# Kernel optimization log

Measured on AMD Instinct MI355X. Metric: run time of the kernel, lower is better.

The kernel has to match this reference:

```python
import jax, jax.numpy as jnp
import numpy as np

N = 100000   # nodes
G = 256      # graphs
E = 120000   # edges per relation
IN = 162
HID = 128
R = 5
L = 2        # extra RGCN layers beyond the initial one


def setup_inputs() -> dict:
    key = jax.random.key(0)
    ks = jax.random.split(key, 24)
    s = 0.05
    inp = {
        "X": jax.random.normal(ks[0], (N, IN), jnp.float32),
        "batch": jnp.sort(jax.random.randint(ks[6], (N,), 0, G)),
    }
    for i in range(R):
        inp[f"edge_index{i+1}"] = jax.random.randint(ks[1 + i], (2, E), 0, N)
    # RGCN initial layer params
    inp["W0"] = jax.random.normal(ks[7], (R, IN, HID), jnp.float32) * s
    inp["root0"] = jax.random.normal(ks[8], (IN, HID), jnp.float32) * s
    inp["b0"] = jnp.zeros((HID,), jnp.float32)
    # stacked params for the L hidden RGCN layers
    inp["Wl"] = jax.random.normal(ks[9], (L, R, HID, HID), jnp.float32) * s
    inp["rootl"] = jax.random.normal(ks[10], (L, HID, HID), jnp.float32) * s
    inp["bl"] = jnp.zeros((L, HID), jnp.float32)
    # classification head
    inp["Wc1"] = jax.random.normal(ks[11], (HID, HID), jnp.float32) * s
    inp["bc1"] = jnp.zeros((HID,), jnp.float32)
    inp["Wc2"] = jax.random.normal(ks[12], (HID, HID), jnp.float32) * s
    inp["bc2"] = jnp.zeros((HID,), jnp.float32)
    inp["Wc3"] = jax.random.normal(ks[13], (HID, 1), jnp.float32) * s
    inp["bc3"] = jnp.zeros((1,), jnp.float32)
    return inp


def _seg_mean(msg, dst, num):
    # scatter-mean over destination nodes (PyG RGCNConv uses aggr='mean' per relation)
    s = jax.ops.segment_sum(msg, dst, num_segments=num)
    c = jax.ops.segment_sum(jnp.ones(msg.shape[0], msg.dtype), dst, num_segments=num)
    return s / jnp.maximum(c, 1.0)[:, None]


def _rgcn(x, W, root, b, src, dst):
    # src, dst: [R, E]; W: [R, d_in, d_out]
    msgs = jnp.einsum("ref,rfh->reh", x[src], W)          # [R, E, HID]
    agg = jax.vmap(_seg_mean, in_axes=(0, 0, None))(msgs, dst, N)  # [R, N, HID]
    return x @ root + b + agg.sum(0)


def reference(X, edge_index1, edge_index2, edge_index3, edge_index4, edge_index5,
              batch, W0, root0, b0, Wl, rootl, bl, Wc1, bc1, Wc2, bc2, Wc3, bc3):
    ei = jnp.stack([edge_index1, edge_index2, edge_index3, edge_index4, edge_index5])  # [R,2,E]
    src, dst = ei[:, 0, :], ei[:, 1, :]
    h = jax.nn.relu(_rgcn(X, W0, root0, b0, src, dst))
    for l in range(L):
        h = jax.nn.relu(_rgcn(h, Wl[l], rootl[l], bl[l], src, dst))
    # mean readout over graphs
    s = jax.ops.segment_sum(h, batch, num_segments=G)
    c = jax.ops.segment_sum(jnp.ones((N,), h.dtype), batch, num_segments=G)
    read = s / jnp.maximum(c, 1.0)[:, None]
    h = jax.nn.relu(read @ Wc1 + bc1)
    h = jax.nn.relu(h @ Wc2 + bc2)
    return h @ Wc3 + bc3
```

## Files before the change

### kernel.cpp

```cpp
#include <hip/hip_runtime.h>

#define N_NODES 100000
#define NPAD    100096
#define NTILES  782
#define G_GRAPHS 256
#define IN_F 162
#define HID 128
#define R_REL 5
#define L_LAYERS 2
#define M5 (R_REL * N_NODES)
#define KSEG0 192
#define KC0   (6 * KSEG0)
#define KC1   (6 * HID)

typedef __attribute__((ext_vector_type(8))) short bf16x8;
typedef __attribute__((ext_vector_type(4))) float f32x4;

__device__ __forceinline__ short f2bf(float f) {
    union { float f; unsigned u; } v; v.f = f;
    unsigned r = (v.u + 0x7fffu + ((v.u >> 16) & 1u)) >> 16;
    return (short)r;
}
__device__ __forceinline__ float bf2f(unsigned short u) {
    union { unsigned u; float f; } v; v.u = ((unsigned)u) << 16;
    return v.f;
}

__global__ void k_count(const int* e0, const int* e1, const int* e2,
                        const int* e3, const int* e4, int* cnt, int E) {
    int gid = blockIdx.x * 256 + threadIdx.x;
    if (gid >= R_REL * E) return;
    int r = gid / E, e = gid - r * E;
    const int* ei = (r == 0) ? e0 : (r == 1) ? e1 : (r == 2) ? e2 : (r == 3) ? e3 : e4;
    atomicAdd(&cnt[r * N_NODES + ei[E + e]], 1);
}

__global__ __launch_bounds__(256) void k_scan1(const int* __restrict__ cnt,
                                               int* __restrict__ off, int* __restrict__ bsum) {
    __shared__ int ts[256];
    int t = threadIdx.x;
    int base = blockIdx.x * 1024 + t * 4;
    int v[4];
    #pragma unroll
    for (int j = 0; j < 4; j++) v[j] = (base + j < M5) ? cnt[base + j] : 0;
    int tsum = v[0] + v[1] + v[2] + v[3];
    ts[t] = tsum; __syncthreads();
    for (int o = 1; o < 256; o <<= 1) {
        int x = (t >= o) ? ts[t - o] : 0;
        __syncthreads();
        ts[t] += x;
        __syncthreads();
    }
    if (t == 255) bsum[blockIdx.x] = ts[255];
    int run = ts[t] - tsum;
    #pragma unroll
    for (int j = 0; j < 4; j++) { if (base + j < M5) off[base + j] = run; run += v[j]; }
}

__global__ __launch_bounds__(512) void k_scan2(int* bsum, int nblk) {
    __shared__ int ts[512];
    int t = threadIdx.x;
    int v = (t < nblk) ? bsum[t] : 0;
    ts[t] = v; __syncthreads();
    for (int o = 1; o < 512; o <<= 1) {
        int x = (t >= o) ? ts[t - o] : 0;
        __syncthreads();
        ts[t] += x;
        __syncthreads();
    }
    if (t < nblk) bsum[t] = ts[t] - v;
}

__global__ void k_scan3(const int* __restrict__ off, const int* __restrict__ bsum,
                        int* __restrict__ mstart, int* __restrict__ mcur,
                        const int* __restrict__ cnt, float* __restrict__ invc) {
    int i = blockIdx.x * 256 + threadIdx.x;
    if (i >= M5) return;
    int o = off[i] + bsum[i >> 10];
    mstart[i] = o;
    mcur[i] = o;
    int c = cnt[i];
    invc[i] = 1.0f / (float)max(c, 1);
    if (i == M5 - 1) mstart[M5] = o + c;
}

__global__ void k_fill(const int* e0, const int* e1, const int* e2,
                       const int* e3, const int* e4, int* mcur,
                       int* __restrict__ mrec, int E) {
    int gid = blockIdx.x * 256 + threadIdx.x;
    if (gid >= R_REL * E) return;
    int r = gid / E, e = gid - r * E;
    const int* ei = (r == 0) ? e0 : (r == 1) ? e1 : (r == 2) ? e2 : (r == 3) ? e3 : e4;
    int src = ei[e], dst = ei[E + e];
    int pos = atomicAdd(&mcur[r * N_NODES + dst], 1);
    mrec[pos] = src;
}

__global__ void k_castX(const float* __restrict__ X, unsigned short* __restrict__ Xb) {
    int gid = blockIdx.x * 256 + threadIdx.x;
    if (gid >= NPAD * KSEG0) return;
    int row = gid / KSEG0, k = gid - row * KSEG0;
    float v = (row < N_NODES && k < IN_F) ? X[(size_t)row * IN_F + k] : 0.f;
    Xb[gid] = (unsigned short)f2bf(v);
}

__global__ void k_tw0(const float* __restrict__ root0, const float* __restrict__ W0,
                      short* __restrict__ out) {
    int gid = blockIdx.x * 256 + threadIdx.x;
    if (gid >= 128 * KC0) return;
    int col = gid / KC0;
    int kk = gid - col * KC0;
    int chunk = kk / KSEG0, k = kk - chunk * KSEG0;
    float v = 0.f;
    if (k < IN_F)
        v = (chunk == 0) ? root0[k * HID + col]
                         : W0[((size_t)(chunk - 1) * IN_F + k) * HID + col];
    out[gid] = f2bf(v);
}

__global__ void k_twl(const float* __restrict__ rootl, const float* __restrict__ Wl,
                      short* __restrict__ out) {
    int gid = blockIdx.x * 256 + threadIdx.x;
    if (gid >= L_LAYERS * 128 * KC1) return;
    int l = gid / (128 * KC1);
    int rem = gid - l * 128 * KC1;
    int col = rem / KC1;
    int kk = rem - col * KC1;
    int chunk = kk / HID, k = kk - chunk * HID;
    float v = (chunk == 0) ? rootl[((size_t)l * HID + k) * HID + col]
                           : Wl[(((size_t)l * R_REL + (chunk - 1)) * HID + k) * HID + col];
    out[gid] = f2bf(v);
}

template<int KSEG>
__global__ __launch_bounds__(256)
void gemm_fused(const unsigned short* __restrict__ A0, const short* __restrict__ Wt,
                const float* __restrict__ bias,
                const int* __restrict__ mstart, const int* __restrict__ mrec,
                const float* __restrict__ invc,
                unsigned short* __restrict__ Hout) {
    constexpr int KS = KSEG / 32;
    constexpr int KCAT = 6 * KSEG;
    constexpr int SA = KSEG + 8;
    constexpr int NP = KSEG / 64;
    __shared__ short Zs[128 * SA];

    const int row0 = blockIdx.x * 128;
    const int tid = threadIdx.x;
    const int lane = tid & 63, wv = tid >> 6;
    const int quad = lane >> 4, l16 = lane & 15;
    const int wr0 = (wv >> 1) * 64, wc0 = (wv & 1) * 64;

    const unsigned short* a0p = A0 + (size_t)(row0 + wr0 + l16) * KSEG + quad * 8;
    const short* Bp = Wt + (size_t)(wc0 + l16) * KCAT + quad * 8;

    f32x4 acc[4][4];
    #pragma unroll
    for (int i = 0; i < 4; i++)
        #pragma unroll
        for (int j = 0; j < 4; j++) acc[i][j] = (f32x4){0.f, 0.f, 0.f, 0.f};

    bf16x8 ac[4], bc[4], an[4], bn[4];
    #pragma unroll
    for (int i = 0; i < 4; i++) {
        ac[i] = *(const bf16x8*)(a0p + (size_t)i * 16 * KSEG);
        bc[i] = *(const bf16x8*)(Bp + (size_t)i * 16 * KCAT);
    }
    #pragma unroll
    for (int t = 0; t < KS; t++) {
        if (t + 1 < KS) {
            #pragma unroll
            for (int i = 0; i < 4; i++) {
                an[i] = *(const bf16x8*)(a0p + (size_t)i * 16 * KSEG + (t + 1) * 32);
                bn[i] = *(const bf16x8*)(Bp + (size_t)i * 16 * KCAT + (t + 1) * 32);
            }
        }
        #pragma unroll
        for (int i = 0; i < 4; i++)
            #pragma unroll
            for (int j = 0; j < 4; j++)
                acc[i][j] = __builtin_amdgcn_mfma_f32_16x16x32_bf16(ac[i], bc[j], acc[i][j], 0, 0, 0);
        if (t + 1 < KS) {
            #pragma unroll
            for (int i = 0; i < 4; i++) { ac[i] = an[i]; bc[i] = bn[i]; }
        }
    }

    for (int sg = 0; sg < R_REL; sg++) {
        const int tb = (1 + sg) * KS;
        #pragma unroll
        for (int j = 0; j < 4; j++)
            bc[j] = *(const bf16x8*)(Bp + (size_t)j * 16 * KCAT + tb * 32);

        const int segbase = sg * N_NODES;
        for (int bt = 0; bt < 8; bt++) {
            const int d = row0 + wv * 32 + bt * 4 + quad;
            int s = 0, e = 0;
            float w = 0.f;
            if (d < N_NODES) {
                s = mstart[segbase + d];
                e = mstart[segbase + d + 1];
                w = invc[segbase + d];
            }
            float s0[NP], s1[NP], s2[NP], s3[NP];
            #pragma unroll
            for (int p = 0; p < NP; p++) { s0[p] = 0.f; s1[p] = 0.f; s2[p] = 0.f; s3[p] = 0.f; }
            int srcn = (s < e) ? mrec[s] : 0;
            for (int j = s; j < e; j++) {
                int src = srcn;
                if (j + 1 < e) srcn = mrec[j + 1];
                const unsigned short* row = A0 + (size_t)src * KSEG;
                #pragma unroll
                for (int p = 0; p < NP; p++) {
                    uint2 v = *(const uint2*)(row + p * 64 + l16 * 4);
                    s0[p] += bf2f((unsigned short)(v.x & 0xffff));
                    s1[p] += bf2f((unsigned short)(v.x >> 16));
                    s2[p] += bf2f((unsigned short)(v.y & 0xffff));
                    s3[p] += bf2f((unsigned short)(v.y >> 16));
                }
            }
            int dl = wv * 32 + bt * 4 + quad;
            #pragma unroll
            for (int p = 0; p < NP; p++) {
                unsigned x = (unsigned)(unsigned short)f2bf(s0[p] * w) |
                             ((unsigned)(unsigned short)f2bf(s1[p] * w) << 16);
                unsigned y = (unsigned)(unsigned short)f2bf(s2[p] * w) |
                             ((unsigned)(unsigned short)f2bf(s3[p] * w) << 16);
                uint2 pv; pv.x = x; pv.y = y;
                *(uint2*)&Zs[dl * SA + p * 64 + l16 * 4] = pv;
            }
        }
        __syncthreads();

        #pragma unroll
        for (int k = 0; k < KS; k++) {
            if (k + 1 < KS) {
                #pragma unroll
                for (int j = 0; j < 4; j++)
                    bn[j] = *(const bf16x8*)(Bp + (size_t)j * 16 * KCAT + (tb + k + 1) * 32);
            }
            #pragma unroll
            for (int i = 0; i < 4; i++)
                ac[i] = *(const bf16x8*)&Zs[(wr0 + i * 16 + l16) * SA + k * 32 + quad * 8];
            #pragma unroll
            for (int i = 0; i < 4; i++)
                #pragma unroll
                for (int j = 0; j < 4; j++)
                    acc[i][j] = __builtin_amdgcn_mfma_f32_16x16x32_bf16(ac[i], bc[j], acc[i][j], 0, 0, 0);
            if (k + 1 < KS) {
                #pragma unroll
                for (int j = 0; j < 4; j++) bc[j] = bn[j];
            }
        }
        __syncthreads();
    }

    float bj[4];
    #pragma unroll
    for (int j = 0; j < 4; j++) bj[j] = bias[wc0 + j * 16 + l16];
    #pragma unroll
    for (int i = 0; i < 4; i++)
        #pragma unroll
        for (int j = 0; j < 4; j++)
            #pragma unroll
            for (int reg = 0; reg < 4; reg++)
                Zs[(wr0 + i * 16 + quad * 4 + reg) * 136 + wc0 + j * 16 + l16] =
                    f2bf(fmaxf(acc[i][j][reg] + bj[j], 0.f));
    __syncthreads();

    #pragma unroll
    for (int s = 0; s < 8; s++) {
        int row = (tid >> 4) + s * 16;
        int col = (tid & 15) * 8;
        bf16x8 v = *(const bf16x8*)&Zs[row * 136 + col];
        *(bf16x8*)&Hout[(size_t)(row0 + row) * HID + col] = v;
    }
}

__global__ __launch_bounds__(128)
void k_pool(const unsigned short* __restrict__ h, const int* __restrict__ batch,
            float* __restrict__ pooled) {
    int c = threadIdx.x;
    int start = blockIdx.x * 128;
    if (start >= N_NODES) return;
    int end = min(start + 128, N_NODES);
    int g = batch[start];
    float s = 0.f;
    for (int i = start; i < end; i++) {
        int gi = batch[i];
        if (gi != g) { atomicAdd(&pooled[g * HID + c], s); s = 0.f; g = gi; }
        s += bf2f(h[(size_t)i * HID + c]);
    }
    atomicAdd(&pooled[g * HID + c], s);
}

__device__ int lower_bound_i(const int* a, int n, int v) {
    int lo = 0, hi = n;
    while (lo < hi) {
        int mid = (lo + hi) >> 1;
        if (a[mid] < v) lo = mid + 1; else hi = mid;
    }
    return lo;
}

__global__ __launch_bounds__(128)
void k_mlp(const float* __restrict__ pooled, const int* __restrict__ batch,
           const float* __restrict__ Wc1, const float* __restrict__ bc1,
           const float* __restrict__ Wc2, const float* __restrict__ bc2,
           const float* __restrict__ Wc3, const float* __restrict__ bc3,
           float* __restrict__ out) {
    int g = blockIdx.x;
    int c = threadIdx.x;
    __shared__ int range[2];
    if (c == 0) range[0] = lower_bound_i(batch, N_NODES, g);
    if (c == 1) range[1] = lower_bound_i(batch, N_NODES, g + 1);
    __syncthreads();
    float denom = fmaxf((float)(range[1] - range[0]), 1.0f);
    __shared__ float row[HID], h1[HID], h2[HID];
    row[c] = pooled[g * HID + c] / denom;
    __syncthreads();
    float acc = bc1[c];
    for (int k = 0; k < HID; k++) acc += row[k] * Wc1[k * HID + c];
    h1[c] = fmaxf(acc, 0.f);
    __syncthreads();
    acc = bc2[c];
    for (int k = 0; k < HID; k++) acc += h1[k] * Wc2[k * HID + c];
    h2[c] = fmaxf(acc, 0.f);
    __syncthreads();
    float t = h2[c] * Wc3[c];
    for (int off = 32; off > 0; off >>= 1) t += __shfl_down(t, off, 64);
    __shared__ float part[2];
    if ((c & 63) == 0) part[c >> 6] = t;
    __syncthreads();
    if (c == 0) out[g] = part[0] + part[1] + bc3[0];
}

extern "C" void kernel_launch(void* const* d_in, const int* in_sizes, int n_in,
                              void* d_out, int out_size, void* d_ws, size_t ws_size,
                              hipStream_t stream) {
    const float* X     = (const float*)d_in[0];
    const int*   batch = (const int*)d_in[1];
    const int*   e0 = (const int*)d_in[2];
    const int*   e1 = (const int*)d_in[3];
    const int*   e2 = (const int*)d_in[4];
    const int*   e3 = (const int*)d_in[5];
    const int*   e4 = (const int*)d_in[6];
    const float* W0    = (const float*)d_in[7];
    const float* root0 = (const float*)d_in[8];
    const float* b0    = (const float*)d_in[9];
    const float* Wl    = (const float*)d_in[10];
    const float* rootl = (const float*)d_in[11];
    const float* bl    = (const float*)d_in[12];
    const float* Wc1   = (const float*)d_in[13];
    const float* bc1   = (const float*)d_in[14];
    const float* Wc2   = (const float*)d_in[15];
    const float* bc2   = (const float*)d_in[16];
    const float* Wc3   = (const float*)d_in[17];
    const float* bc3   = (const float*)d_in[18];
    const int E = in_sizes[2] / 2;
    const int NE = R_REL * E;

    char* base = (char*)d_ws;
    size_t o = 0;
    auto carve = [&](size_t bytes) -> char* {
        char* p = base + o;
        o = (o + bytes + 255) & ~(size_t)255;
        return p;
    };
    unsigned short* h1 = (unsigned short*)carve((size_t)NPAD * HID * 2);
    unsigned short* Xb = (unsigned short*)carve((size_t)NPAD * KSEG0 * 2);
    int*   cnt    = (int*)carve((size_t)M5 * 4);
    float* invc   = (float*)carve((size_t)M5 * 4);
    int*   offsc  = (int*)carve((size_t)M5 * 4);
    int*   mstart = (int*)carve((size_t)(M5 + 1) * 4);
    int*   mrec   = (int*)carve((size_t)NE * 4);
    int*   bsum   = (int*)carve(2048);
    float* pooled = (float*)carve((size_t)G_GRAPHS * HID * 4);
    short* Wt0    = (short*)carve((size_t)128 * KC0 * 2);
    short* Wtl    = (short*)carve((size_t)L_LAYERS * 128 * KC1 * 2);
    int*   mcur   = offsc;
    unsigned short* h2 = Xb;

    hipMemsetAsync(cnt, 0, (size_t)M5 * 4, stream);
    hipMemsetAsync(pooled, 0, (size_t)G_GRAPHS * HID * 4, stream);
    int eg = (NE + 255) / 256;
    k_count<<<eg, 256, 0, stream>>>(e0, e1, e2, e3, e4, cnt, E);
    int nblk = (M5 + 1023) / 1024;
    k_scan1<<<nblk, 256, 0, stream>>>(cnt, offsc, bsum);
    k_scan2<<<1, 512, 0, stream>>>(bsum, nblk);
    k_scan3<<<(M5 + 255) / 256, 256, 0, stream>>>(offsc, bsum, mstart, mcur, cnt, invc);
    k_fill<<<eg, 256, 0, stream>>>(e0, e1, e2, e3, e4, mcur, mrec, E);
    k_castX<<<(NPAD * KSEG0 + 255) / 256, 256, 0, stream>>>(X, Xb);
    k_tw0<<<(128 * KC0 + 255) / 256, 256, 0, stream>>>(root0, W0, Wt0);
    k_twl<<<(L_LAYERS * 128 * KC1 + 255) / 256, 256, 0, stream>>>(rootl, Wl, Wtl);

    gemm_fused<KSEG0><<<NTILES, 256, 0, stream>>>(Xb, Wt0, b0, mstart, mrec, invc, h1);
    gemm_fused<HID><<<NTILES, 256, 0, stream>>>(h1, Wtl, bl, mstart, mrec, invc, h2);
    gemm_fused<HID><<<NTILES, 256, 0, stream>>>(h2, Wtl + (size_t)128 * KC1, bl + HID,
                                                mstart, mrec, invc, h1);

    k_pool<<<(N_NODES + 127) / 128, 128, 0, stream>>>(h1, batch, pooled);
    k_mlp<<<G_GRAPHS, 128, 0, stream>>>(pooled, batch, Wc1, bc1, Wc2, bc2, Wc3, bc3, (float*)d_out);
}
```

Measured before the change: 829.3 us.

## Stage CSR offsets and edge indices in LDS and pipeline the neighbour gather

Per-block CSR start offsets and inverse counts for all five relations are preloaded into shared memory, along with each relation's edge-source list (up to 512 entries). Each lane group now walks one contiguous edge range covering 8 destinations, instead of a separate loop per destination. Neighbour-row loads are prefetched two edges ahead, which targets the global index-load latency and short-loop overhead in the gather. The LDS row stride is reduced and stores skip the padded feature columns, and one barrier per relation is removed; this leaves some padding columns uninitialized, which relies on the corresponding weights being zero.

```diff
diff --git a/kernel.cpp b/kernel.cpp
--- a/kernel.cpp
+++ b/kernel.cpp
@@ -141,15 +141,30 @@
                 unsigned short* __restrict__ Hout) {
     constexpr int KS = KSEG / 32;
     constexpr int KCAT = 6 * KSEG;
-    constexpr int SA = KSEG + 8;
+    constexpr int SA = (KSEG == 192) ? 184 : 136;
     constexpr int NP = KSEG / 64;
-    __shared__ short Zs[128 * SA];
+    constexpr int EBUF = 512;
+    __shared__ short Zs[128 * SA + 16];
+    __shared__ int   sMS[5 * 129];
+    __shared__ float sMW[5 * 128];
+    __shared__ int   sE[EBUF];
 
     const int row0 = blockIdx.x * 128;
     const int tid = threadIdx.x;
     const int lane = tid & 63, wv = tid >> 6;
     const int quad = lane >> 4, l16 = lane & 15;
     const int wr0 = (wv >> 1) * 64, wc0 = (wv & 1) * 64;
+    const int local0 = wv * 32 + quad * 8;
+
+    for (int i = tid; i < 5 * 129; i += 256) {
+        int seg = i / 129, o = i - seg * 129;
+        sMS[i] = mstart[seg * N_NODES + min(row0 + o, N_NODES)];
+    }
+    for (int i = tid; i < 5 * 128; i += 256) {
+        int seg = i >> 7, o = i & 127;
+        int d = row0 + o;
+        sMW[i] = (d < N_NODES) ? invc[seg * N_NODES + d] : 0.f;
+    }
 
     const unsigned short* a0p = A0 + (size_t)(row0 + wr0 + l16) * KSEG + quad * 8;
     const short* Bp = Wt + (size_t)(wc0 + l16) * KCAT + quad * 8;
@@ -185,6 +200,7 @@
             for (int i = 0; i < 4; i++) { ac[i] = an[i]; bc[i] = bn[i]; }
         }
     }
+    __syncthreads();
 
     for (int sg = 0; sg < R_REL; sg++) {
         const int tb = (1 + sg) * KS;
@@ -192,42 +208,72 @@
         for (int j = 0; j < 4; j++)
             bc[j] = *(const bf16x8*)(Bp + (size_t)j * 16 * KCAT + tb * 32);
 
-        const int segbase = sg * N_NODES;
-        for (int bt = 0; bt < 8; bt++) {
-            const int d = row0 + wv * 32 + bt * 4 + quad;
-            int s = 0, e = 0;
-            float w = 0.f;
-            if (d < N_NODES) {
-                s = mstart[segbase + d];
-                e = mstart[segbase + d + 1];
-                w = invc[segbase + d];
-            }
-            float s0[NP], s1[NP], s2[NP], s3[NP];
-            #pragma unroll
-            for (int p = 0; p < NP; p++) { s0[p] = 0.f; s1[p] = 0.f; s2[p] = 0.f; s3[p] = 0.f; }
-            int srcn = (s < e) ? mrec[s] : 0;
-            for (int j = s; j < e; j++) {
-                int src = srcn;
-                if (j + 1 < e) srcn = mrec[j + 1];
-                const unsigned short* row = A0 + (size_t)src * KSEG;
+        const int blo = sMS[sg * 129];
+        {
+            int cnt = sMS[sg * 129 + 128] - blo;
+            if (cnt > EBUF) cnt = EBUF;
+            for (int i = tid; i < cnt; i += 256) sE[i] = mrec[blo + i];
+        }
+        __syncthreads();
+
+        {
+            const int jlo = sMS[sg * 129 + local0];
+            const int jhi = sMS[sg * 129 + local0 + 8];
+            int di = 0;
+            int nextb = sMS[sg * 129 + local0 + 1];
+            float a0[NP], a1[NP], a2[NP], a3[NP];
+            #pragma unroll
+            for (int p = 0; p < NP; p++) { a0[p] = 0.f; a1[p] = 0.f; a2[p] = 0.f; a3[p] = 0.f; }
+            uint2 v0[NP], v1[NP];
+            if (jlo < jhi) {
+                int jj = jlo - blo;
+                int src = (jj < EBUF) ? sE[jj] : mrec[jlo];
+                const unsigned short* r = A0 + (size_t)src * KSEG;
+                #pragma unroll
+                for (int p = 0; p < NP; p++) v0[p] = *(const uint2*)(r + p * 64 + l16 * 4);
+            }
+            if (jlo + 1 < jhi) {
+                int jj = jlo + 1 - blo;
+                int src = (jj < EBUF) ? sE[jj] : mrec[jlo + 1];
+                const unsigned short* r = A0 + (size_t)src * KSEG;
+                #pragma unroll
+                for (int p = 0; p < NP; p++) v1[p] = *(const uint2*)(r + p * 64 + l16 * 4);
+            }
+            for (int j = jlo; ; j++) {
+                while (di < 8 && j == nextb) {
+                    float w = sMW[sg * 128 + local0 + di];
+                    int zr = (local0 + di) * SA;
+                    #pragma unroll
+                    for (int p = 0; p < NP; p++) {
+                        unsigned x = (unsigned)(unsigned short)f2bf(a0[p] * w) |
+                                     ((unsigned)(unsigned short)f2bf(a1[p] * w) << 16);
+                        unsigned y = (unsigned)(unsigned short)f2bf(a2[p] * w) |
+                                     ((unsigned)(unsigned short)f2bf(a3[p] * w) << 16);
+                        uint2 pv; pv.x = x; pv.y = y;
+                        if (p < 2 || l16 < 10)
+                            *(uint2*)&Zs[zr + p * 64 + l16 * 4] = pv;
+                        a0[p] = 0.f; a1[p] = 0.f; a2[p] = 0.f; a3[p] = 0.f;
+                    }
+                    di++;
+                    nextb = (di < 8) ? sMS[sg * 129 + local0 + di + 1] : 0x7fffffff;
+                }
+                if (j >= jhi) break;
                 #pragma unroll
                 for (int p = 0; p < NP; p++) {
-                    uint2 v = *(const uint2*)(row + p * 64 + l16 * 4);
-                    s0[p] += bf2f((unsigned short)(v.x & 0xffff));
-                    s1[p] += bf2f((unsigned short)(v.x >> 16));
-                    s2[p] += bf2f((unsigned short)(v.y & 0xffff));
-                    s3[p] += bf2f((unsigned short)(v.y >> 16));
+                    a0[p] += bf2f((unsigned short)(v0[p].x & 0xffff));
+                    a1[p] += bf2f((unsigned short)(v0[p].x >> 16));
+                    a2[p] += bf2f((unsigned short)(v0[p].y & 0xffff));
+                    a3[p] += bf2f((unsigned short)(v0[p].y >> 16));
                 }
-            }
-            int dl = wv * 32 + bt * 4 + quad;
-            #pragma unroll
-            for (int p = 0; p < NP; p++) {
-                unsigned x = (unsigned)(unsigned short)f2bf(s0[p] * w) |
-                             ((unsigned)(unsigned short)f2bf(s1[p] * w) << 16);
-                unsigned y = (unsigned)(unsigned short)f2bf(s2[p] * w) |
-                             ((unsigned)(unsigned short)f2bf(s3[p] * w) << 16);
-                uint2 pv; pv.x = x; pv.y = y;
-                *(uint2*)&Zs[dl * SA + p * 64 + l16 * 4] = pv;
+                #pragma unroll
+                for (int p = 0; p < NP; p++) v0[p] = v1[p];
+                if (j + 2 < jhi) {
+                    int jj = j + 2 - blo;
+                    int src = (jj < EBUF) ? sE[jj] : mrec[j + 2];
+                    const unsigned short* r = A0 + (size_t)src * KSEG;
+                    #pragma unroll
+                    for (int p = 0; p < NP; p++) v1[p] = *(const uint2*)(r + p * 64 + l16 * 4);
+                }
             }
         }
         __syncthreads();
@@ -252,8 +298,8 @@
                 for (int j = 0; j < 4; j++) bc[j] = bn[j];
             }
         }
-        __syncthreads();
-    }
+    }
+    __syncthreads();
 
     float bj[4];
     #pragma unroll
```

Result: faster. 752.1 us (-9.3%).
